# Performance work log

Measured on AMD Instinct MI355X. Metric: run time of the kernel, lower is better.

The kernel has to match this reference:

```python
import jax, jax.numpy as jnp
import numpy as np

B, N, F_IN, E, TOPK = 64, 1024, 64, 128, 32
NEG_SLOPE = 0.2  # GAT leaky-relu slope


def setup_inputs() -> dict:
    key = jax.random.key(0)
    ks = jax.random.split(key, 7)
    x = jax.random.normal(ks[0], (B, N, F_IN), dtype=jnp.float32)
    emb = jax.random.normal(ks[1], (N, E), dtype=jnp.float32)            # nn.Embedding table
    W_fe = jax.random.normal(ks[2], (F_IN, E), dtype=jnp.float32) / np.sqrt(F_IN).astype(np.float32)
    a_src = jax.random.normal(ks[3], (2 * E,), dtype=jnp.float32) * 0.05
    a_dst = jax.random.normal(ks[4], (2 * E,), dtype=jnp.float32) * 0.05
    lin_W = jax.random.normal(ks[5], (E, 1), dtype=jnp.float32) / np.sqrt(E).astype(np.float32)
    lin_b = jnp.zeros((1,), dtype=jnp.float32)
    return {"x": x, "emb": emb, "W_fe": W_fe, "a_src": a_src, "a_dst": a_dst,
            "lin_W": lin_W, "lin_b": lin_b}


def reference(x, emb, W_fe, a_src, a_dst, lin_W, lin_b):
    b, n, _ = x.shape
    e_dim = emb.shape[-1]
    # --- cosine-similarity topk graph construction (shared across batch) ---
    norm = jnp.linalg.norm(emb, axis=-1, keepdims=True)                  # [N,1]
    sim = (emb @ emb.T) / (norm @ norm.T)                                # [N,N]
    idx = jax.lax.top_k(sim, TOPK)[1]                                    # [N,K] int32 neighbor (target) nodes
    # --- graph attention feature extraction ---
    h = jnp.einsum('bnf,fe->bne', x, W_fe)                               # [B,N,E] projected node features
    g = jnp.concatenate([h, jnp.broadcast_to(emb, (b, n, e_dim))], -1)   # [B,N,2E] feat || embedding
    e_s = g @ a_src                                                      # [B,N] source attention term
    e_d = g @ a_dst                                                      # [B,N] target attention term
    # edges: source i repeated TOPK times -> targets idx[i]; softmax over each node's K neighbors
    scores = jax.nn.leaky_relu(e_s[:, :, None] + e_d[:, idx], NEG_SLOPE)  # [B,N,K]
    alpha = jax.nn.softmax(scores, axis=-1)                              # [B,N,K]
    h_dst = h[:, idx, :]                                                 # [B,N,K,E] gathered neighbor feats
    out = jnp.einsum('bnk,bnke->bne', alpha, h_dst)                      # aggregate messages
    out = jax.nn.relu(out)
    # --- linear readout ---
    y = out @ lin_W + lin_b                                              # [B,N,1]
    return y[..., 0]                                                     # [B,N]
```

## Files before the change

### kernel.cpp

```cpp
#include <hip/hip_runtime.h>
#include <math.h>

#define BB 64
#define NN 1024
#define F_IN 64
#define EE 128
#define TOPK 32
#define NEG_SLOPE 0.2f

typedef unsigned int uint;
typedef unsigned short ushort;
typedef unsigned long long ull;
typedef __attribute__((ext_vector_type(8))) short short8;
typedef __attribute__((ext_vector_type(4))) float f32x4;
typedef __attribute__((ext_vector_type(2))) float f32x2;

static __device__ __forceinline__ uint f2bf(float f) {
  const uint x = __float_as_uint(f);
  return (x + 0x7fffu + ((x >> 16) & 1u)) >> 16;
}
static __device__ __forceinline__ float bf_lo(uint u) {
  return __uint_as_float(u << 16);
}
static __device__ __forceinline__ float bf_hi_raw(uint u) {
  return __uint_as_float(u);
}
static __device__ __forceinline__ uint fmono(float f) {
  uint u = __float_as_uint(f);
  return (u & 0x80000000u) ? ~u : (u | 0x80000000u);
}
static __device__ __forceinline__ ull umax64(ull a, ull b) {
  return a > b ? a : b;
}
static __device__ __forceinline__ ull umin64(ull a, ull b) {
  return a < b ? a : b;
}
static __device__ __forceinline__ ull shfl_xor64(ull v, int mask) {
  const uint lo = __shfl_xor((uint)v, mask);
  const uint hi = __shfl_xor((uint)(v >> 32), mask);
  return ((ull)hi << 32) | lo;
}

__global__ __launch_bounds__(256) void k2a_sim(
    const float* __restrict__ emb, const float* __restrict__ a_src,
    const float* __restrict__ a_dst, const float* __restrict__ W_fe,
    uint* __restrict__ keys, float* __restrict__ u_src,
    float* __restrict__ u_dst, ushort* __restrict__ wt,
    float* __restrict__ rn) {
  __shared__ __align__(16) uint eni[16 * 64];
  __shared__ __align__(16) uint enj[256 * 64];
  const int t = threadIdx.x, wid = t >> 6, lane = t & 63;
  const int it = blockIdx.x >> 2, js = blockIdx.x & 3;
  const int i0 = it * 16, jw0 = js * 256;

  const int rh = t >> 1, h = t & 1;
#pragma unroll
  for (int p = 0; p < 2; ++p) {
    const int r = p * 128 + rh;
    const float* src = emb + (size_t)(jw0 + r) * EE + h * 64;
    float4 v[16];
#pragma unroll
    for (int q = 0; q < 16; ++q) v[q] = *(const float4*)&src[q * 4];
    float sq = 0.f;
#pragma unroll
    for (int q = 0; q < 16; ++q)
      sq += v[q].x * v[q].x + v[q].y * v[q].y + v[q].z * v[q].z +
            v[q].w * v[q].w;
    sq += __shfl_xor(sq, 1);
    const float rs = rsqrtf(sq);
    if (it == 0 && h == 0) rn[jw0 + r] = rs;
    char* dst = (char*)(enj + r * 64);
    const int swz = (r & 7) << 4;
#pragma unroll
    for (int s16 = 0; s16 < 8; ++s16) {
      const float4 a = v[s16 * 2], b2 = v[s16 * 2 + 1];
      uint4 w4;
      w4.x = f2bf(a.x * rs) | (f2bf(a.y * rs) << 16);
      w4.y = f2bf(a.z * rs) | (f2bf(a.w * rs) << 16);
      w4.z = f2bf(b2.x * rs) | (f2bf(b2.y * rs) << 16);
      w4.w = f2bf(b2.z * rs) | (f2bf(b2.w * rs) << 16);
      *(uint4*)(dst + ((h * 128 + s16 * 16) ^ swz)) = w4;
    }
  }
  if (t < 32) {
    const int r = t >> 1, hh = t & 1;
    const float* src = emb + (size_t)(i0 + r) * EE + hh * 64;
    float4 v[16];
#pragma unroll
    for (int q = 0; q < 16; ++q) v[q] = *(const float4*)&src[q * 4];
    float sq = 0.f;
#pragma unroll
    for (int q = 0; q < 16; ++q)
      sq += v[q].x * v[q].x + v[q].y * v[q].y + v[q].z * v[q].z +
            v[q].w * v[q].w;
    sq += __shfl_xor(sq, 1);
    const float rs = rsqrtf(sq);
    char* dst = (char*)(eni + r * 64);
    const int swz = (r & 7) << 4;
#pragma unroll
    for (int s16 = 0; s16 < 8; ++s16) {
      const float4 a = v[s16 * 2], b2 = v[s16 * 2 + 1];
      uint4 w4;
      w4.x = f2bf(a.x * rs) | (f2bf(a.y * rs) << 16);
      w4.y = f2bf(a.z * rs) | (f2bf(a.w * rs) << 16);
      w4.z = f2bf(b2.x * rs) | (f2bf(b2.y * rs) << 16);
      w4.w = f2bf(b2.z * rs) | (f2bf(b2.w * rs) << 16);
      *(uint4*)(dst + ((hh * 128 + s16 * 16) ^ swz)) = w4;
    }
  }
  __syncthreads();

  const int nn = lane & 15, quad = lane >> 4;
  short8 af[4];
#pragma unroll
  for (int s = 0; s < 4; ++s) {
    const int kb = (s * 64 + quad * 16) ^ ((nn & 7) << 4);
    af[s] = *(const short8*)((const char*)eni + nn * 256 + kb);
  }
  f32x4 acc[4];
#pragma unroll
  for (int t4 = 0; t4 < 4; ++t4) acc[t4] = (f32x4){0.f, 0.f, 0.f, 0.f};
#pragma unroll
  for (int t4 = 0; t4 < 4; ++t4) {
    const int rloc = wid * 64 + t4 * 16 + nn;
    const char* brow = (const char*)enj + rloc * 256;
    const int swz = (rloc & 7) << 4;
#pragma unroll
    for (int s = 0; s < 4; ++s) {
      const short8 bf = *(const short8*)(brow + ((s * 64 + quad * 16) ^ swz));
      acc[t4] =
          __builtin_amdgcn_mfma_f32_16x16x32_bf16(af[s], bf, acc[t4], 0, 0, 0);
    }
  }
#pragma unroll
  for (int t4 = 0; t4 < 4; ++t4) {
    const int j = jw0 + wid * 64 + t4 * 16 + nn;
#pragma unroll
    for (int reg = 0; reg < 4; ++reg) {
      const int i = i0 + quad * 4 + reg;
      keys[(size_t)i * NN + j] = fmono(acc[t4][reg]);
    }
  }

  if (js == 0) {
#pragma unroll
    for (int rr = 0; rr < 4; ++rr) {
      const int row = i0 + wid * 4 + rr;
      const float* er = emb + (size_t)row * EE;
      const float e0 = er[lane], e1 = er[64 + lane];
      float us = e0 * a_src[EE + lane] + e1 * a_src[EE + 64 + lane];
      float ud = e0 * a_dst[EE + lane] + e1 * a_dst[EE + 64 + lane];
#pragma unroll
      for (int o = 1; o <= 32; o <<= 1) {
        us += __shfl_xor(us, o);
        ud += __shfl_xor(ud, o);
      }
      if (lane == 0) {
        u_src[row] = us;
        u_dst[row] = ud;
      }
    }
  } else if (js == 1 && it < 32) {
    const int g = it * 256 + t;
    const int n = g >> 6, k = g & 63;
    wt[g] = (ushort)f2bf(W_fe[k * EE + n]);
  }
}

__global__ __launch_bounds__(256) void k23(
    const uint* __restrict__ keys, int* __restrict__ idx_out,
    const float* __restrict__ x, const ushort* __restrict__ wt,
    const float* __restrict__ a_src, const float* __restrict__ a_dst,
    const float* __restrict__ u_src, const float* __restrict__ u_dst,
    uint* __restrict__ h2, float* __restrict__ es, float* __restrict__ ed,
    const float* __restrict__ emb, const float* __restrict__ rn) {
  __shared__ ull cand[256];
  __shared__ float rowbuf[EE];
  const int t = threadIdx.x, wid = t >> 6, lane = t & 63;

  if (blockIdx.x < NN) {
    const int row = blockIdx.x;
    if (t < EE) rowbuf[t] = emb[(size_t)row * EE + t];

    const int jb = wid * 256 + lane * 4;
    const uint4 kv = *(const uint4*)&keys[(size_t)row * NN + jb];
    ull xr[4];
    xr[0] = ((ull)kv.x << 32) | (uint)(jb + 0);
    xr[1] = ((ull)kv.y << 32) | (uint)(jb + 1);
    xr[2] = ((ull)kv.z << 32) | (uint)(jb + 2);
    xr[3] = ((ull)kv.w << 32) | (uint)(jb + 3);

#pragma unroll
    for (int k = 2; k <= 256; k <<= 1) {
#pragma unroll
      for (int d = 128; d >= 1; d >>= 1) {
        if (d > (k >> 1)) continue;
        if (d >= 4) {
          const int pl = d >> 2;
          const bool lower = (lane & pl) == 0;
#pragma unroll
          for (int r = 0; r < 4; ++r) {
            const ull o = shfl_xor64(xr[r], pl);
            const bool desc = (((lane * 4 + r) & k) == 0);
            const bool keepmax = (desc == lower);
            xr[r] = keepmax ? umax64(xr[r], o) : umin64(xr[r], o);
          }
        } else if (d == 2) {
#pragma unroll
          for (int r = 0; r < 2; ++r) {
            const bool desc = (((lane * 4 + r) & k) == 0);
            const ull hi = umax64(xr[r], xr[r + 2]);
            const ull lo = umin64(xr[r], xr[r + 2]);
            xr[r] = desc ? hi : lo;
            xr[r + 2] = desc ? lo : hi;
          }
        } else {
#pragma unroll
          for (int r = 0; r < 4; r += 2) {
            const bool desc = (((lane * 4 + r) & k) == 0);
            const ull hi = umax64(xr[r], xr[r + 1]);
            const ull lo = umin64(xr[r], xr[r + 1]);
            xr[r] = desc ? hi : lo;
            xr[r + 1] = desc ? lo : hi;
          }
        }
      }
    }
    if (lane < 16) {
#pragma unroll
      for (int r = 0; r < 4; ++r) cand[wid * 64 + lane * 4 + r] = xr[r];
    }
    __syncthreads();

    if (wid < 2) {
      const ull a0 = cand[(2 * wid) * 64 + lane];
      const ull a1 = cand[(2 * wid) * 64 + 64 + 63 - lane];
      ull v0 = umax64(a0, a1);
#pragma unroll
      for (int d = 32; d >= 1; d >>= 1) {
        const ull o = shfl_xor64(v0, d);
        v0 = ((lane & d) == 0) ? umax64(v0, o) : umin64(v0, o);
      }
      cand[wid * 128 + lane] = v0;
    }
    __syncthreads();

    if (wid == 0) {
      const ull a0 = cand[lane];
      const ull a1 = cand[128 + 63 - lane];
      ull v0 = umax64(a0, a1);
#pragma unroll
      for (int d = 32; d >= 1; d >>= 1) {
        const ull o = shfl_xor64(v0, d);
        v0 = ((lane & d) == 0) ? umax64(v0, o) : umin64(v0, o);
      }
      cand[192 + lane] = v0 & 1023u;
    }
    __syncthreads();

    const int c = t >> 2, dq = t & 3;
    const int jc = (int)(uint)cand[192 + c];
    const float* ej = emb + (size_t)jc * EE + dq * 32;
    const float* rb = rowbuf + dq * 32;
    float dot = 0.f;
#pragma unroll
    for (int q = 0; q < 8; ++q) {
      const float4 a = *(const float4*)&ej[q * 4];
      const float4 b = *(const float4*)&rb[q * 4];
      dot += a.x * b.x + a.y * b.y + a.z * b.z + a.w * b.w;
    }
    dot += __shfl_xor(dot, 1);
    dot += __shfl_xor(dot, 2);
    if (dq == 0) {
      const float cosv = dot * rn[row] * rn[jc];
      cand[c] = ((ull)fmono(cosv) << 32) | (uint)jc;
    }
    __syncthreads();

    if (wid == 0) {
      ull v = cand[lane];
#pragma unroll
      for (int k = 2; k <= 64; k <<= 1) {
#pragma unroll
        for (int d0 = 32; d0 >= 1; d0 >>= 1) {
          if (d0 > (k >> 1)) continue;
          const ull o = shfl_xor64(v, d0);
          const bool up = (lane & k) == 0;
          v = (up == ((lane & d0) == 0)) ? umax64(v, o) : umin64(v, o);
        }
      }
      if (lane < 32) idx_out[(size_t)row * TOPK + lane] = (int)(v & 1023u);
    }
  } else {
    const int row0 = (blockIdx.x - NN) * 64;
    const int nn = lane & 15, quad = lane >> 4;
    const int row0w = row0 + wid * 16;

    short8 af[2];
#pragma unroll
    for (int s = 0; s < 2; ++s) {
      const float* xr2 = x + (size_t)(row0w + nn) * F_IN + s * 32 + quad * 8;
      const float4 v0 = *(const float4*)&xr2[0];
      const float4 v1 = *(const float4*)&xr2[4];
      af[s][0] = (short)f2bf(v0.x);
      af[s][1] = (short)f2bf(v0.y);
      af[s][2] = (short)f2bf(v0.z);
      af[s][3] = (short)f2bf(v0.w);
      af[s][4] = (short)f2bf(v1.x);
      af[s][5] = (short)f2bf(v1.y);
      af[s][6] = (short)f2bf(v1.z);
      af[s][7] = (short)f2bf(v1.w);
    }

    f32x4 acc[8];
#pragma unroll
    for (int T = 0; T < 8; ++T) acc[T] = (f32x4){0.f, 0.f, 0.f, 0.f};

#pragma unroll
    for (int T = 0; T < 8; ++T) {
#pragma unroll
      for (int s = 0; s < 2; ++s) {
        const short8 bf =
            *(const short8*)&wt[(T * 16 + nn) * F_IN + s * 32 + quad * 8];
        acc[T] =
            __builtin_amdgcn_mfma_f32_16x16x32_bf16(af[s], bf, acc[T], 0, 0, 0);
      }
    }

    const int growbase = row0w + quad * 4;
#pragma unroll
    for (int reg = 0; reg < 4; ++reg) {
      uint* hr = h2 + (size_t)(growbase + reg) * 64 + nn;
#pragma unroll
      for (int T4 = 0; T4 < 4; ++T4) {
        hr[T4 * 16] =
            f2bf(acc[2 * T4][reg]) | (f2bf(acc[2 * T4 + 1][reg]) << 16);
      }
    }
    float ae[8], de[8];
#pragma unroll
    for (int T = 0; T < 8; ++T) {
      ae[T] = a_src[T * 16 + nn];
      de[T] = a_dst[T * 16 + nn];
    }
#pragma unroll
    for (int reg = 0; reg < 4; ++reg) {
      float ps = 0.f, pd = 0.f;
#pragma unroll
      for (int T = 0; T < 8; ++T) {
        ps += acc[T][reg] * ae[T];
        pd += acc[T][reg] * de[T];
      }
#pragma unroll
      for (int o = 1; o <= 8; o <<= 1) {
        ps += __shfl_xor(ps, o);
        pd += __shfl_xor(pd, o);
      }
      if (nn == 0) {
        const int grow = growbase + reg;
        const int node = grow & (NN - 1);
        es[grow] = ps + u_src[node];
        ed[grow] = pd + u_dst[node];
      }
    }
  }
}

__global__ __launch_bounds__(256) void k4_attn(
    const uint* __restrict__ h2, const float* __restrict__ es,
    const float* __restrict__ ed, const int* __restrict__ idx,
    const float* __restrict__ lin_W, const float* __restrict__ lin_b,
    float* __restrict__ y) {
  const int t = threadIdx.x, wid = t >> 6, lane = t & 63;
  const int blk = blockIdx.x;
  const int xcd = blk & 7, x = blk >> 3;
  const int b = xcd * 8 + (x >> 6);
  const int q = lane >> 4, ll = lane & 15;
  const int n = (x & 63) * 16 + wid * 4 + q;
  const int pbase = q * 64;

  const float* edb = ed + (size_t)b * NN;
  const float* esb = es + (size_t)b * NN;
  const char* hb = (const char*)(h2 + (size_t)b * NN * 64);

  const int j0 = idx[n * TOPK + ll];
  const int j1 = idx[n * TOPK + 16 + ll];
  const int off0 = j0 << 8, off1 = j1 << 8;
  int offA[16], offB[16];
#pragma unroll
  for (int k = 0; k < 16; ++k) {
    offA[k] = __builtin_amdgcn_ds_bpermute(pbase + k * 4, off0);
    offB[k] = __builtin_amdgcn_ds_bpermute(pbase + k * 4, off1);
  }
  float4 tvA[16];
#pragma unroll
  for (int k = 0; k < 16; ++k)
    tvA[k] = *(const float4*)(hb + ((uint)offA[k] + ll * 16));
  float4 tvB[16];
#pragma unroll
  for (int k = 0; k < 16; ++k)
    tvB[k] = *(const float4*)(hb + ((uint)offB[k] + ll * 16));

  const float esv = esb[n];
  float s0 = esv + edb[j0];
  float s1 = esv + edb[j1];
  s0 = s0 > 0.f ? s0 : NEG_SLOPE * s0;
  s1 = s1 > 0.f ? s1 : NEG_SLOPE * s1;
  const float p0 = __expf(s0);
  const float p1 = __expf(s1);
  float dsum = p0 + p1;
#pragma unroll
  for (int o = 1; o <= 8; o <<= 1) dsum += __shfl_xor(dsum, o);
  const float rs = 1.0f / dsum;
  const float w0 = p0 * rs, w1 = p1 * rs;
  float wkA[16], wkB[16];
#pragma unroll
  for (int k = 0; k < 16; ++k) {
    wkA[k] = __uint_as_float(
        __builtin_amdgcn_ds_bpermute(pbase + k * 4, __float_as_uint(w0)));
    wkB[k] = __uint_as_float(
        __builtin_amdgcn_ds_bpermute(pbase + k * 4, __float_as_uint(w1)));
  }

  float lwlo[4], lwhi[4];
#pragma unroll
  for (int i = 0; i < 4; ++i) {
    const int c = 4 * ll + i;
    const int t4 = c >> 4, nn2 = c & 15;
    lwlo[i] = lin_W[t4 * 32 + nn2];
    lwhi[i] = lin_W[t4 * 32 + 16 + nn2];
  }
  const float bias = lin_b[0];

  f32x2 accA = {0.f, 0.f}, accB = {0.f, 0.f};
  f32x2 accC = {0.f, 0.f}, accD = {0.f, 0.f};

#pragma unroll
  for (int k = 0; k < 16; ++k) {
    const float ak = wkA[k];
    const float4 u = tvA[k];
    f32x2 wp;
    wp.x = ak;
    wp.y = ak;
    f32x2 hi01, hi23, lo01, lo23;
    hi01.x = u.x;
    hi01.y = u.y;
    hi23.x = u.z;
    hi23.y = u.w;
    lo01.x = bf_lo(__float_as_uint(u.x));
    lo01.y = bf_lo(__float_as_uint(u.y));
    lo23.x = bf_lo(__float_as_uint(u.z));
    lo23.y = bf_lo(__float_as_uint(u.w));
    asm("v_pk_fma_f32 %0, %1, %2, %0" : "+v"(accA) : "v"(lo01), "v"(wp));
    asm("v_pk_fma_f32 %0, %1, %2, %0" : "+v"(accB) : "v"(hi01), "v"(wp));
    asm("v_pk_fma_f32 %0, %1, %2, %0" : "+v"(accC) : "v"(lo23), "v"(wp));
    asm("v_pk_fma_f32 %0, %1, %2, %0" : "+v"(accD) : "v"(hi23), "v"(wp));
  }
#pragma unroll
  for (int k = 0; k < 16; ++k) {
    const float ak = wkB[k];
    const float4 u = tvB[k];
    f32x2 wp;
    wp.x = ak;
    wp.y = ak;
    f32x2 hi01, hi23, lo01, lo23;
    hi01.x = u.x;
    hi01.y = u.y;
    hi23.x = u.z;
    hi23.y = u.w;
    lo01.x = bf_lo(__float_as_uint(u.x));
    lo01.y = bf_lo(__float_as_uint(u.y));
    lo23.x = bf_lo(__float_as_uint(u.z));
    lo23.y = bf_lo(__float_as_uint(u.w));
    asm("v_pk_fma_f32 %0, %1, %2, %0" : "+v"(accA) : "v"(lo01), "v"(wp));
    asm("v_pk_fma_f32 %0, %1, %2, %0" : "+v"(accB) : "v"(hi01), "v"(wp));
    asm("v_pk_fma_f32 %0, %1, %2, %0" : "+v"(accC) : "v"(lo23), "v"(wp));
    asm("v_pk_fma_f32 %0, %1, %2, %0" : "+v"(accD) : "v"(hi23), "v"(wp));
  }

  float r = fmaxf(accA.x, 0.f) * lwlo[0] + fmaxf(accA.y, 0.f) * lwlo[1] +
            fmaxf(accB.x, 0.f) * lwhi[0] + fmaxf(accB.y, 0.f) * lwhi[1] +
            fmaxf(accC.x, 0.f) * lwlo[2] + fmaxf(accC.y, 0.f) * lwlo[3] +
            fmaxf(accD.x, 0.f) * lwhi[2] + fmaxf(accD.y, 0.f) * lwhi[3];
#pragma unroll
  for (int o = 1; o <= 8; o <<= 1) r += __shfl_xor(r, o);
  if (ll == 0) y[(size_t)b * NN + n] = r + bias;
}

extern "C" void kernel_launch(void* const* d_in, const int* in_sizes, int n_in,
                              void* d_out, int out_size, void* d_ws,
                              size_t ws_size, hipStream_t stream) {
  const float* x = (const float*)d_in[0];
  const float* emb = (const float*)d_in[1];
  const float* W_fe = (const float*)d_in[2];
  const float* a_src = (const float*)d_in[3];
  const float* a_dst = (const float*)d_in[4];
  const float* lin_W = (const float*)d_in[5];
  const float* lin_b = (const float*)d_in[6];
  float* y = (float*)d_out;

  char* ws = (char*)d_ws;
  float* rn = (float*)(ws + 0);
  float* u_src = (float*)(ws + 4096);
  float* u_dst = (float*)(ws + 8192);
  int* idx = (int*)(ws + 16384);
  float* es = (float*)(ws + 147456);
  float* ed = (float*)(ws + 409600);
  uint* h2 = (uint*)(ws + 671744);
  uint* keys = (uint*)(ws + 17448960);
  ushort* wt = (ushort*)(ws + 21643264);

  k2a_sim<<<256, 256, 0, stream>>>(emb, a_src, a_dst, W_fe, keys, u_src,
                                   u_dst, wt, rn);
  k23<<<2048, 256, 0, stream>>>(keys, idx, x, wt, a_src, a_dst, u_src, u_dst,
                                h2, es, ed, emb, rn);
  k4_attn<<<4096, 256, 0, stream>>>(h2, es, ed, idx, lin_W, lin_b, y);
}
```

Before: 127.7 us.

## Stage per-batch feature half in LDS and gather neighbors from shared memory

The attention kernel now loads one batch's half of the bf16 feature table (1024 nodes × 64 features) into 128KB of LDS, then gathers all 32 neighbors per node from LDS instead of issuing random global loads. Each block covers 512 nodes for one feature half. The two halves' partial readouts are combined with atomicAdd into y, which is pre-initialized to the bias in the previous kernel. The grid shrinks to 256 blocks at one block per CU. In exchange it adds atomics and redundant softmax work across the two halves, and occupancy drops to a single block per CU.

```diff
diff --git a/kernel.cpp b/kernel.cpp
--- a/kernel.cpp
+++ b/kernel.cpp
@@ -173,7 +173,8 @@
     const float* __restrict__ a_src, const float* __restrict__ a_dst,
     const float* __restrict__ u_src, const float* __restrict__ u_dst,
     uint* __restrict__ h2, float* __restrict__ es, float* __restrict__ ed,
-    const float* __restrict__ emb, const float* __restrict__ rn) {
+    const float* __restrict__ emb, const float* __restrict__ rn,
+    float* __restrict__ y, const float* __restrict__ lin_b) {
   __shared__ ull cand[256];
   __shared__ float rowbuf[EE];
   const int t = threadIdx.x, wid = t >> 6, lane = t & 63;
@@ -343,6 +344,7 @@
       ae[T] = a_src[T * 16 + nn];
       de[T] = a_dst[T * 16 + nn];
     }
+    const float bias = lin_b[0];
 #pragma unroll
     for (int reg = 0; reg < 4; ++reg) {
       float ps = 0.f, pd = 0.f;
@@ -361,130 +363,110 @@
         const int node = grow & (NN - 1);
         es[grow] = ps + u_src[node];
         ed[grow] = pd + u_dst[node];
-      }
-    }
-  }
-}
-
-__global__ __launch_bounds__(256) void k4_attn(
+        y[grow] = bias;
+      }
+    }
+  }
+}
+
+#define JV(K)                                             \
+  (((K) & 3) == 0   ? jv[(K) >> 2].x                      \
+   : ((K) & 3) == 1 ? jv[(K) >> 2].y                      \
+   : ((K) & 3) == 2 ? jv[(K) >> 2].z                      \
+                    : jv[(K) >> 2].w)
+
+__global__ __launch_bounds__(256, 1) void k4_attn(
     const uint* __restrict__ h2, const float* __restrict__ es,
     const float* __restrict__ ed, const int* __restrict__ idx,
     const float* __restrict__ lin_W, const float* __restrict__ lin_b,
     float* __restrict__ y) {
+  __shared__ __align__(16) uint hs[NN * 32];
   const int t = threadIdx.x, wid = t >> 6, lane = t & 63;
-  const int blk = blockIdx.x;
-  const int xcd = blk & 7, x = blk >> 3;
-  const int b = xcd * 8 + (x >> 6);
-  const int q = lane >> 4, ll = lane & 15;
-  const int n = (x & 63) * 16 + wid * 4 + q;
-  const int pbase = q * 64;
-
+  const int o = lane >> 3, sub = lane & 7;
+  const int g = blockIdx.x;
+  const int q = (g & 7) * 16 + (g >> 4);
+  const int nh = (g >> 3) & 1;
+  const int b = q >> 1, dh = q & 1;
+
+  const uint* hb = h2 + (size_t)b * NN * 64;
   const float* edb = ed + (size_t)b * NN;
   const float* esb = es + (size_t)b * NN;
-  const char* hb = (const char*)(h2 + (size_t)b * NN * 64);
-
-  const int j0 = idx[n * TOPK + ll];
-  const int j1 = idx[n * TOPK + 16 + ll];
-  const int off0 = j0 << 8, off1 = j1 << 8;
-  int offA[16], offB[16];
-#pragma unroll
-  for (int k = 0; k < 16; ++k) {
-    offA[k] = __builtin_amdgcn_ds_bpermute(pbase + k * 4, off0);
-    offB[k] = __builtin_amdgcn_ds_bpermute(pbase + k * 4, off1);
-  }
-  float4 tvA[16];
-#pragma unroll
-  for (int k = 0; k < 16; ++k)
-    tvA[k] = *(const float4*)(hb + ((uint)offA[k] + ll * 16));
-  float4 tvB[16];
-#pragma unroll
-  for (int k = 0; k < 16; ++k)
-    tvB[k] = *(const float4*)(hb + ((uint)offB[k] + ll * 16));
-
-  const float esv = esb[n];
-  float s0 = esv + edb[j0];
-  float s1 = esv + edb[j1];
-  s0 = s0 > 0.f ? s0 : NEG_SLOPE * s0;
-  s1 = s1 > 0.f ? s1 : NEG_SLOPE * s1;
-  const float p0 = __expf(s0);
-  const float p1 = __expf(s1);
-  float dsum = p0 + p1;
-#pragma unroll
-  for (int o = 1; o <= 8; o <<= 1) dsum += __shfl_xor(dsum, o);
-  const float rs = 1.0f / dsum;
-  const float w0 = p0 * rs, w1 = p1 * rs;
-  float wkA[16], wkB[16];
-#pragma unroll
-  for (int k = 0; k < 16; ++k) {
-    wkA[k] = __uint_as_float(
-        __builtin_amdgcn_ds_bpermute(pbase + k * 4, __float_as_uint(w0)));
-    wkB[k] = __uint_as_float(
-        __builtin_amdgcn_ds_bpermute(pbase + k * 4, __float_as_uint(w1)));
-  }
+
+#pragma unroll
+  for (int i = 0; i < 32; ++i) {
+    const int j = wid * 256 + i * 8 + o;
+    const uint4 v = *(const uint4*)(hb + (size_t)j * 64 + dh * 32 + sub * 4);
+    *(uint4*)(hs + j * 32 + sub * 4) = v;
+  }
+  __syncthreads();
 
   float lwlo[4], lwhi[4];
 #pragma unroll
   for (int i = 0; i < 4; ++i) {
-    const int c = 4 * ll + i;
-    const int t4 = c >> 4, nn2 = c & 15;
-    lwlo[i] = lin_W[t4 * 32 + nn2];
-    lwhi[i] = lin_W[t4 * 32 + 16 + nn2];
-  }
-  const float bias = lin_b[0];
-
-  f32x2 accA = {0.f, 0.f}, accB = {0.f, 0.f};
-  f32x2 accC = {0.f, 0.f}, accD = {0.f, 0.f};
-
-#pragma unroll
-  for (int k = 0; k < 16; ++k) {
-    const float ak = wkA[k];
-    const float4 u = tvA[k];
-    f32x2 wp;
-    wp.x = ak;
-    wp.y = ak;
-    f32x2 hi01, hi23, lo01, lo23;
-    hi01.x = u.x;
-    hi01.y = u.y;
-    hi23.x = u.z;
-    hi23.y = u.w;
-    lo01.x = bf_lo(__float_as_uint(u.x));
-    lo01.y = bf_lo(__float_as_uint(u.y));
-    lo23.x = bf_lo(__float_as_uint(u.z));
-    lo23.y = bf_lo(__float_as_uint(u.w));
-    asm("v_pk_fma_f32 %0, %1, %2, %0" : "+v"(accA) : "v"(lo01), "v"(wp));
-    asm("v_pk_fma_f32 %0, %1, %2, %0" : "+v"(accB) : "v"(hi01), "v"(wp));
-    asm("v_pk_fma_f32 %0, %1, %2, %0" : "+v"(accC) : "v"(lo23), "v"(wp));
-    asm("v_pk_fma_f32 %0, %1, %2, %0" : "+v"(accD) : "v"(hi23), "v"(wp));
-  }
-#pragma unroll
-  for (int k = 0; k < 16; ++k) {
-    const float ak = wkB[k];
-    const float4 u = tvB[k];
-    f32x2 wp;
-    wp.x = ak;
-    wp.y = ak;
-    f32x2 hi01, hi23, lo01, lo23;
-    hi01.x = u.x;
-    hi01.y = u.y;
-    hi23.x = u.z;
-    hi23.y = u.w;
-    lo01.x = bf_lo(__float_as_uint(u.x));
-    lo01.y = bf_lo(__float_as_uint(u.y));
-    lo23.x = bf_lo(__float_as_uint(u.z));
-    lo23.y = bf_lo(__float_as_uint(u.w));
-    asm("v_pk_fma_f32 %0, %1, %2, %0" : "+v"(accA) : "v"(lo01), "v"(wp));
-    asm("v_pk_fma_f32 %0, %1, %2, %0" : "+v"(accB) : "v"(hi01), "v"(wp));
-    asm("v_pk_fma_f32 %0, %1, %2, %0" : "+v"(accC) : "v"(lo23), "v"(wp));
-    asm("v_pk_fma_f32 %0, %1, %2, %0" : "+v"(accD) : "v"(hi23), "v"(wp));
-  }
-
-  float r = fmaxf(accA.x, 0.f) * lwlo[0] + fmaxf(accA.y, 0.f) * lwlo[1] +
-            fmaxf(accB.x, 0.f) * lwhi[0] + fmaxf(accB.y, 0.f) * lwhi[1] +
-            fmaxf(accC.x, 0.f) * lwlo[2] + fmaxf(accC.y, 0.f) * lwlo[3] +
-            fmaxf(accD.x, 0.f) * lwhi[2] + fmaxf(accD.y, 0.f) * lwhi[3];
-#pragma unroll
-  for (int o = 1; o <= 8; o <<= 1) r += __shfl_xor(r, o);
-  if (ll == 0) y[(size_t)b * NN + n] = r + bias;
+    const int u = dh * 32 + sub * 4 + i;
+    const int T4 = u >> 4, nn2 = u & 15;
+    lwlo[i] = lin_W[T4 * 32 + nn2];
+    lwhi[i] = lin_W[T4 * 32 + 16 + nn2];
+  }
+
+  for (int it = 0; it < 16; ++it) {
+    const int n = nh * 512 + wid * 128 + it * 8 + o;
+    const int* ir = idx + n * TOPK;
+    int4 jv[8];
+#pragma unroll
+    for (int qq = 0; qq < 8; ++qq) jv[qq] = *(const int4*)(ir + qq * 4);
+
+    float4 tv[32];
+#pragma unroll
+    for (int k = 0; k < 32; ++k)
+      tv[k] = *(const float4*)(hs + JV(k) * 32 + sub * 4);
+    __builtin_amdgcn_sched_barrier(0);
+
+    const float esv = esb[n];
+    float p[32];
+    float dsum = 0.f;
+#pragma unroll
+    for (int k = 0; k < 32; ++k) {
+      float s = esv + edb[JV(k)];
+      s = s > 0.f ? s : NEG_SLOPE * s;
+      p[k] = __expf(s);
+      dsum += p[k];
+    }
+    const float rs = 1.0f / dsum;
+
+    f32x2 accA = {0.f, 0.f}, accB = {0.f, 0.f};
+    f32x2 accC = {0.f, 0.f}, accD = {0.f, 0.f};
+#pragma unroll
+    for (int k = 0; k < 32; ++k) {
+      const float wk = p[k] * rs;
+      const float4 u = tv[k];
+      f32x2 wp;
+      wp.x = wk;
+      wp.y = wk;
+      f32x2 hi01, hi23, lo01, lo23;
+      hi01.x = u.x;
+      hi01.y = u.y;
+      hi23.x = u.z;
+      hi23.y = u.w;
+      lo01.x = bf_lo(__float_as_uint(u.x));
+      lo01.y = bf_lo(__float_as_uint(u.y));
+      lo23.x = bf_lo(__float_as_uint(u.z));
+      lo23.y = bf_lo(__float_as_uint(u.w));
+      asm("v_pk_fma_f32 %0, %1, %2, %0" : "+v"(accA) : "v"(lo01), "v"(wp));
+      asm("v_pk_fma_f32 %0, %1, %2, %0" : "+v"(accB) : "v"(hi01), "v"(wp));
+      asm("v_pk_fma_f32 %0, %1, %2, %0" : "+v"(accC) : "v"(lo23), "v"(wp));
+      asm("v_pk_fma_f32 %0, %1, %2, %0" : "+v"(accD) : "v"(hi23), "v"(wp));
+    }
+
+    float r = fmaxf(accA.x, 0.f) * lwlo[0] + fmaxf(accA.y, 0.f) * lwlo[1] +
+              fmaxf(accB.x, 0.f) * lwhi[0] + fmaxf(accB.y, 0.f) * lwhi[1] +
+              fmaxf(accC.x, 0.f) * lwlo[2] + fmaxf(accC.y, 0.f) * lwlo[3] +
+              fmaxf(accD.x, 0.f) * lwhi[2] + fmaxf(accD.y, 0.f) * lwhi[3];
+    r += __shfl_xor(r, 1);
+    r += __shfl_xor(r, 2);
+    r += __shfl_xor(r, 4);
+    if (sub == 0) atomicAdd(&y[(size_t)b * NN + n], r);
+  }
 }
 
 extern "C" void kernel_launch(void* const* d_in, const int* in_sizes, int n_in,
@@ -513,6 +495,6 @@
   k2a_sim<<<256, 256, 0, stream>>>(emb, a_src, a_dst, W_fe, keys, u_src,
                                    u_dst, wt, rn);
   k23<<<2048, 256, 0, stream>>>(keys, idx, x, wt, a_src, a_dst, u_src, u_dst,
-                                h2, es, ed, emb, rn);
-  k4_attn<<<4096, 256, 0, stream>>>(h2, es, ed, idx, lin_W, lin_b, y);
-}
+                                h2, es, ed, emb, rn, y, lin_b);
+  k4_attn<<<256, 256, 0, stream>>>(h2, es, ed, idx, lin_W, lin_b, y);
+}
```

Result: slower. 149.7 us (+17.3%).
